# Kernel optimization log

Measured on AMD Instinct MI355X. Metric: run time of the kernel, lower is better.

## Reference

```python
import jax, jax.numpy as jnp
import numpy as np

N_NODES = 100000
N_EDGES = 1600000
IN_CH = 128
OUT_CH = 128


def setup_inputs() -> dict:
    key = jax.random.key(0)
    k1, k2, k3 = jax.random.split(key, 3)
    x = jax.random.normal(k1, (N_NODES, IN_CH), dtype=jnp.float32)
    edge_index = jax.random.randint(k2, (2, N_EDGES), 0, N_NODES, dtype=jnp.int64)
    # Glorot-style init like PyG GCNConv
    W = jax.random.normal(k3, (IN_CH, OUT_CH), dtype=jnp.float32) * (1.0 / np.sqrt(IN_CH))
    b = jnp.zeros((OUT_CH,), dtype=jnp.float32)
    return {"x": x, "edge_index": edge_index, "W": W, "b": b}


def reference(x, edge_index, W, b):
    N = x.shape[0]
    # add self-loops (PyG GCNConv default add_self_loops=True)
    loop = jnp.arange(N, dtype=edge_index.dtype)
    src = jnp.concatenate([edge_index[0], loop])
    dst = jnp.concatenate([edge_index[1], loop])
    # symmetric normalization: deg computed over destination (col)
    deg = jax.ops.segment_sum(jnp.ones_like(src, dtype=x.dtype), dst, num_segments=N)
    dinv = jnp.where(deg > 0, jax.lax.rsqrt(deg), 0.0)
    norm = dinv[src] * dinv[dst]  # [E+N]
    xw = x @ W  # [N, out_ch]
    msg = xw[src] * norm[:, None]  # gather + scale, [E+N, out_ch]
    out = jax.ops.segment_sum(msg, dst, num_segments=N) + b  # scatter-add
    return jax.nn.relu(out)
```

## Files before the change

### kernel.cpp

```cpp
#include <hip/hip_runtime.h>
#include <hip/hip_bf16.h>

constexpr int CH    = 128;
constexpr int BSH   = 7;
constexpr int CAPSH = 12;
constexpr int CHUNK = 6250;
constexpr int CHCAP = 6400;

typedef __attribute__((ext_vector_type(8))) short short8v;
typedef __attribute__((ext_vector_type(4))) float f32x4;

__device__ __forceinline__ unsigned short f2bf(float f) {
    unsigned u = __float_as_uint(f);
    u = (u + 0x7fffu + ((u >> 16) & 1u)) >> 16;
    return (unsigned short)u;
}

__global__ __launch_bounds__(256) void k_bin(const int* __restrict__ src,
                                             const int* __restrict__ dst, int E,
                                             int* __restrict__ bucket_cnt,
                                             unsigned* __restrict__ packed,
                                             const float* __restrict__ W,
                                             unsigned short* __restrict__ Wt) {
    __shared__ int hist[1024];
    __shared__ int start[1024];
    __shared__ int cursor[1024];
    __shared__ int gofs[1024];
    __shared__ int tscan[256];
    __shared__ unsigned       sorted[CHCAP];
    __shared__ unsigned short sbkt[CHCAP];

    int t = threadIdx.x;
    if (blockIdx.x < 32) {
        int idx = blockIdx.x * 256 + t;
        int c  = idx & 127;
        int k2 = (idx >> 7) * 2;
        unsigned pk = (unsigned)f2bf(W[(size_t)k2 * CH + c]) |
                      ((unsigned)f2bf(W[(size_t)(k2 + 1) * CH + c]) << 16);
        *(unsigned*)(Wt + (size_t)c * CH + k2) = pk;
    }
    #pragma unroll
    for (int i = 0; i < 4; ++i) hist[t + i * 256] = 0;
    __syncthreads();

    int e0 = blockIdx.x * CHUNK;
    int e1 = min(e0 + CHUNK, E);
    for (int e = e0 + t; e < e1; e += 256)
        atomicAdd(&hist[dst[e] >> BSH], 1);
    __syncthreads();
    int b4 = t * 4;
    int c0 = hist[b4], c1 = hist[b4 + 1], c2 = hist[b4 + 2], c3 = hist[b4 + 3];
    int tsum = c0 + c1 + c2 + c3;
    tscan[t] = tsum;
    __syncthreads();
    for (int off = 1; off < 256; off <<= 1) {
        int v = (t >= off) ? tscan[t - off] : 0;
        __syncthreads();
        tscan[t] += v;
        __syncthreads();
    }
    int eb = tscan[t] - tsum;
    start[b4]     = eb;
    start[b4 + 1] = eb + c0;
    start[b4 + 2] = eb + c0 + c1;
    start[b4 + 3] = eb + c0 + c1 + c2;
    cursor[b4]     = eb;
    cursor[b4 + 1] = eb + c0;
    cursor[b4 + 2] = eb + c0 + c1;
    cursor[b4 + 3] = eb + c0 + c1 + c2;
    __syncthreads();
    #pragma unroll
    for (int i = 0; i < 4; ++i) {
        int b = t + i * 256;
        int c = hist[b];
        gofs[b] = (c > 0) ? atomicAdd(&bucket_cnt[b], c) : 0;
    }
    __syncthreads();
    for (int e = e0 + t; e < e1; e += 256) {
        int d = dst[e];
        int b = d >> BSH;
        int pos = atomicAdd(&cursor[b], 1);
        sorted[pos] = (unsigned)src[e] | ((unsigned)(d & ((1 << BSH) - 1)) << 20);
        sbkt[pos] = (unsigned short)b;
    }
    __syncthreads();
    int nloc = e1 - e0;
    for (int i = t; i < nloc; i += 256) {
        int b = sbkt[i];
        int gpos = (b << CAPSH) + gofs[b] + (i - start[b]);
        packed[gpos] = sorted[i];
    }
}

__global__ __launch_bounds__(256) void k_bucket(const int* __restrict__ bucket_cnt,
                                                const unsigned* __restrict__ packed,
                                                int* __restrict__ eidx,
                                                uint2* __restrict__ rowinfo,
                                                float* __restrict__ dinv, int N) {
    __shared__ int fh[128];
    __shared__ int fs[128];
    __shared__ int fc[128];
    int b = blockIdx.x;
    int t = threadIdx.x;
    int cnt = bucket_cnt[b];
    if (t < 128) fh[t] = 0;
    __syncthreads();
    const unsigned* pk = packed + ((size_t)b << CAPSH);
    for (int i = t; i < cnt; i += 256)
        atomicAdd(&fh[(pk[i] >> 20) & 127], 1);
    __syncthreads();
    if (t < 128) fs[t] = fh[t];
    __syncthreads();
    for (int off = 1; off < 128; off <<= 1) {
        int v = 0;
        if (t < 128 && t >= off) v = fs[t - off];
        __syncthreads();
        if (t < 128) fs[t] += v;
        __syncthreads();
    }
    if (t < 128) {
        int excl = fs[t] - fh[t];
        fc[t] = excl;
        int node = (b << BSH) + t;
        if (node < N) {
            rowinfo[node] = make_uint2((unsigned)((b << CAPSH) + excl), (unsigned)fh[t]);
            dinv[node] = rsqrtf((float)fh[t] + 1.0f);
        }
    }
    __syncthreads();
    int* eo = eidx + ((size_t)b << CAPSH);
    for (int i = t; i < cnt; i += 256) {
        unsigned p = pk[i];
        int f = (p >> 20) & 127;
        int pos = atomicAdd(&fc[f], 1);
        eo[pos] = (int)(p & 0xFFFFF);
    }
}

__global__ __launch_bounds__(256) void k_gemm(const float* __restrict__ x,
                                              const unsigned short* __restrict__ Wt,
                                              const float* __restrict__ dinv,
                                              unsigned short* __restrict__ xwb, int N) {
    __shared__ __align__(16) unsigned short xs[64 * CH];
    int t = threadIdx.x;
    int w = t >> 6, lane = t & 63;
    int c16 = lane & 15, kq = lane >> 4, kb = kq * 8;
    int row0 = blockIdx.x * 64;
    int arow = row0 + w * 16 + c16;
    bool av = arow < N;
    const float* xp = x + (size_t)(av ? arow : 0) * CH;

    f32x4 acc[8];
    #pragma unroll
    for (int f = 0; f < 8; ++f) acc[f] = (f32x4){0.f, 0.f, 0.f, 0.f};

    #pragma unroll
    for (int kc = 0; kc < 4; ++kc) {
        float4 x0 = make_float4(0.f, 0.f, 0.f, 0.f), x1 = x0;
        if (av) {
            x0 = ((const float4*)(xp + kc * 32 + kb))[0];
            x1 = ((const float4*)(xp + kc * 32 + kb))[1];
        }
        union { short8v v; __hip_bfloat162 h[4]; } au;
        au.h[0] = __float22bfloat162_rn(make_float2(x0.x, x0.y));
        au.h[1] = __float22bfloat162_rn(make_float2(x0.z, x0.w));
        au.h[2] = __float22bfloat162_rn(make_float2(x1.x, x1.y));
        au.h[3] = __float22bfloat162_rn(make_float2(x1.z, x1.w));
        #pragma unroll
        for (int f = 0; f < 8; ++f) {
            short8v b = *(const short8v*)(Wt + (size_t)(f * 16 + c16) * CH + kc * 32 + kb);
            acc[f] = __builtin_amdgcn_mfma_f32_16x16x32_bf16(au.v, b, acc[f], 0, 0, 0);
        }
    }

    #pragma unroll
    for (int r = 0; r < 4; ++r) {
        int row_l = w * 16 + kq * 4 + r;
        int grow  = row0 + row_l;
        float dv  = (grow < N) ? dinv[grow] : 0.f;
        #pragma unroll
        for (int f = 0; f < 8; ++f) {
            int col = f * 16 + c16;
            unsigned bo = ((unsigned)((row_l * CH + col) * 2)) ^ ((unsigned)(row_l & 7) << 4);
            *(unsigned short*)((char*)xs + bo) = f2bf(acc[f][r] * dv);
        }
    }
    __syncthreads();
    #pragma unroll
    for (int i = 0; i < 4; ++i) {
        int g = i * 256 + t;
        int row_l = g >> 4;
        unsigned bo = ((unsigned)(g * 16)) ^ ((unsigned)(row_l & 7) << 4);
        uint4 v = *(const uint4*)((const char*)xs + bo);
        int row = row0 + row_l;
        if (row < N) ((uint4*)(xwb + (size_t)row * CH))[g & 15] = v;
    }
}

__global__ __launch_bounds__(256) void k_gather(const uint2* __restrict__ rowinfo,
                                                const int* __restrict__ eidx,
                                                const unsigned short* __restrict__ xwb,
                                                const float* __restrict__ dinv,
                                                const float* __restrict__ bias,
                                                float* __restrict__ out, int N) {
    int n = blockIdx.x * 4 + (threadIdx.x >> 6);
    if (n >= N) return;
    int lane = threadIdx.x & 63;
    int q    = lane >> 4;
    int c16  = lane & 15;
    uint2 ri = rowinfo[n];
    int beg = (int)ri.x;
    int deg = (int)ri.y;
    float acc[8];
    #pragma unroll
    for (int i = 0; i < 8; ++i) acc[i] = 0.f;

    const uint4* xw4 = (const uint4*)xwb;
    for (int p0 = 0; p0 < deg; p0 += 64) {
        int m = deg - p0; if (m > 64) m = 64;
        int myi = 0;
        if (lane < m) myi = eidx[beg + p0 + lane];
        int jj = q;
        int s  = (jj < m) ? __shfl(myi, jj & 63) : N;
        uint4 u = xw4[(size_t)s * 16 + c16];
        for (int j = 4; j < m; j += 4) {
            int jj2 = j + q;
            int ss  = __shfl(myi, jj2 & 63);
            int s2  = (jj2 < m) ? ss : N;
            uint4 u2 = xw4[(size_t)s2 * 16 + c16];
            acc[0] += __uint_as_float(u.x << 16);
            acc[1] += __uint_as_float(u.x & 0xffff0000u);
            acc[2] += __uint_as_float(u.y << 16);
            acc[3] += __uint_as_float(u.y & 0xffff0000u);
            acc[4] += __uint_as_float(u.z << 16);
            acc[5] += __uint_as_float(u.z & 0xffff0000u);
            acc[6] += __uint_as_float(u.w << 16);
            acc[7] += __uint_as_float(u.w & 0xffff0000u);
            u = u2;
        }
        acc[0] += __uint_as_float(u.x << 16);
        acc[1] += __uint_as_float(u.x & 0xffff0000u);
        acc[2] += __uint_as_float(u.y << 16);
        acc[3] += __uint_as_float(u.y & 0xffff0000u);
        acc[4] += __uint_as_float(u.z << 16);
        acc[5] += __uint_as_float(u.z & 0xffff0000u);
        acc[6] += __uint_as_float(u.w << 16);
        acc[7] += __uint_as_float(u.w & 0xffff0000u);
    }
    #pragma unroll
    for (int i = 0; i < 8; ++i) {
        acc[i] += __shfl_xor(acc[i], 16);
        acc[i] += __shfl_xor(acc[i], 32);
    }
    if (lane < 16) {
        float dn = dinv[n];
        uint4 u = xw4[(size_t)n * 16 + c16];
        acc[0] += __uint_as_float(u.x << 16);
        acc[1] += __uint_as_float(u.x & 0xffff0000u);
        acc[2] += __uint_as_float(u.y << 16);
        acc[3] += __uint_as_float(u.y & 0xffff0000u);
        acc[4] += __uint_as_float(u.z << 16);
        acc[5] += __uint_as_float(u.z & 0xffff0000u);
        acc[6] += __uint_as_float(u.w << 16);
        acc[7] += __uint_as_float(u.w & 0xffff0000u);
        float4 b0 = ((const float4*)bias)[c16 * 2];
        float4 b1 = ((const float4*)bias)[c16 * 2 + 1];
        float4 o0, o1;
        o0.x = fmaxf(fmaf(acc[0], dn, b0.x), 0.f);
        o0.y = fmaxf(fmaf(acc[1], dn, b0.y), 0.f);
        o0.z = fmaxf(fmaf(acc[2], dn, b0.z), 0.f);
        o0.w = fmaxf(fmaf(acc[3], dn, b0.w), 0.f);
        o1.x = fmaxf(fmaf(acc[4], dn, b1.x), 0.f);
        o1.y = fmaxf(fmaf(acc[5], dn, b1.y), 0.f);
        o1.z = fmaxf(fmaf(acc[6], dn, b1.z), 0.f);
        o1.w = fmaxf(fmaf(acc[7], dn, b1.w), 0.f);
        ((float4*)(out + (size_t)n * CH))[c16 * 2]     = o0;
        ((float4*)(out + (size_t)n * CH))[c16 * 2 + 1] = o1;
    }
}

extern "C" void kernel_launch(void* const* d_in, const int* in_sizes, int n_in,
                              void* d_out, int out_size, void* d_ws, size_t ws_size,
                              hipStream_t stream) {
    const float* x  = (const float*)d_in[0];
    const int*   ei = (const int*)d_in[1];
    const float* W  = (const float*)d_in[2];
    const float* b  = (const float*)d_in[3];

    int N = in_sizes[0] / CH;
    int E = in_sizes[1] / 2;
    const int* src = ei;
    const int* dst = ei + E;
    float* out = (float*)d_out;

    int nbuck = (N + (1 << BSH) - 1) >> BSH;
    size_t nslots = (size_t)nbuck << CAPSH;

    auto al = [](uintptr_t p) { return (p + 255) & ~(uintptr_t)255; };
    uintptr_t base = (uintptr_t)d_ws;
    unsigned short* xwb = (unsigned short*)base;
    int* bucket_cnt = (int*)(xwb + (size_t)(N + 1) * CH);
    uintptr_t p = al((uintptr_t)(bucket_cnt + nbuck));
    uint2* rowinfo  = (uint2*)p;               p = al(p + (size_t)N * 8);
    float* dinv     = (float*)p;               p = al(p + (size_t)N * 4);
    unsigned short* Wt = (unsigned short*)p;   p = al(p + (size_t)CH * CH * 2);
    unsigned* packed   = (unsigned*)p;         p = al(p + nslots * 4);
    int* eidx          = (int*)p;

    int nbin = (E + CHUNK - 1) / CHUNK;

    hipMemsetAsync(xwb + (size_t)N * CH, 0, (size_t)CH * 2 + (size_t)nbuck * 4, stream);
    k_bin   <<<nbin, 256, 0, stream>>>(src, dst, E, bucket_cnt, packed, W, Wt);
    k_bucket<<<nbuck, 256, 0, stream>>>(bucket_cnt, packed, eidx, rowinfo, dinv, N);
    k_gemm  <<<(N + 63) / 64, 256, 0, stream>>>(x, Wt, dinv, xwb, N);
    k_gather<<<(N + 3) / 4, 256, 0, stream>>>(rowinfo, eidx, xwb, dinv, b, out, N);
}
```

Before: 154.4 us.

## Split gather by column slices across blocks so each lane handles more edges

The gather kernel now splits the 128 output channels into 8 slices of 16, each handled by a separate block (blockIdx & 7). Within a wave, lane pairs cover a 16-channel slice, so 32 edges are fetched in parallel instead of 4, and each wave processes 4 nodes in sequence. The intent is to raise memory-level parallelism for the random row gathers and to use packed 2-wide float adds. The cost is that each edge index list is read 8 times, each gathered request is only 16 bytes, and the cross-lane reduction grows to 5 shuffle stages.

```diff
diff --git a/kernel.cpp b/kernel.cpp
--- a/kernel.cpp
+++ b/kernel.cpp
@@ -9,6 +9,7 @@
 
 typedef __attribute__((ext_vector_type(8))) short short8v;
 typedef __attribute__((ext_vector_type(4))) float f32x4;
+typedef __attribute__((ext_vector_type(2))) float f32x2;
 
 __device__ __forceinline__ unsigned short f2bf(float f) {
     unsigned u = __float_as_uint(f);
@@ -197,85 +198,75 @@
     }
 }
 
+#define ACCP(U) \
+    acc0 += (f32x2){__uint_as_float((U).x << 16), __uint_as_float((U).x & 0xffff0000u)}; \
+    acc1 += (f32x2){__uint_as_float((U).y << 16), __uint_as_float((U).y & 0xffff0000u)}; \
+    acc2 += (f32x2){__uint_as_float((U).z << 16), __uint_as_float((U).z & 0xffff0000u)}; \
+    acc3 += (f32x2){__uint_as_float((U).w << 16), __uint_as_float((U).w & 0xffff0000u)};
+
 __global__ __launch_bounds__(256) void k_gather(const uint2* __restrict__ rowinfo,
                                                 const int* __restrict__ eidx,
                                                 const unsigned short* __restrict__ xwb,
                                                 const float* __restrict__ dinv,
                                                 const float* __restrict__ bias,
                                                 float* __restrict__ out, int N) {
-    int n = blockIdx.x * 4 + (threadIdx.x >> 6);
-    if (n >= N) return;
-    int lane = threadIdx.x & 63;
-    int q    = lane >> 4;
-    int c16  = lane & 15;
-    uint2 ri = rowinfo[n];
-    int beg = (int)ri.x;
-    int deg = (int)ri.y;
-    float acc[8];
-    #pragma unroll
-    for (int i = 0; i < 8; ++i) acc[i] = 0.f;
-
+    int s    = blockIdx.x & 7;
+    int g    = blockIdx.x >> 3;
+    int tid  = threadIdx.x;
+    int lane = tid & 63;
+    int wv   = tid >> 6;
+    int eh   = lane >> 1;
+    int half = lane & 1;
     const uint4* xw4 = (const uint4*)xwb;
-    for (int p0 = 0; p0 < deg; p0 += 64) {
-        int m = deg - p0; if (m > 64) m = 64;
-        int myi = 0;
-        if (lane < m) myi = eidx[beg + p0 + lane];
-        int jj = q;
-        int s  = (jj < m) ? __shfl(myi, jj & 63) : N;
-        uint4 u = xw4[(size_t)s * 16 + c16];
-        for (int j = 4; j < m; j += 4) {
-            int jj2 = j + q;
-            int ss  = __shfl(myi, jj2 & 63);
-            int s2  = (jj2 < m) ? ss : N;
-            uint4 u2 = xw4[(size_t)s2 * 16 + c16];
-            acc[0] += __uint_as_float(u.x << 16);
-            acc[1] += __uint_as_float(u.x & 0xffff0000u);
-            acc[2] += __uint_as_float(u.y << 16);
-            acc[3] += __uint_as_float(u.y & 0xffff0000u);
-            acc[4] += __uint_as_float(u.z << 16);
-            acc[5] += __uint_as_float(u.z & 0xffff0000u);
-            acc[6] += __uint_as_float(u.w << 16);
-            acc[7] += __uint_as_float(u.w & 0xffff0000u);
-            u = u2;
-        }
-        acc[0] += __uint_as_float(u.x << 16);
-        acc[1] += __uint_as_float(u.x & 0xffff0000u);
-        acc[2] += __uint_as_float(u.y << 16);
-        acc[3] += __uint_as_float(u.y & 0xffff0000u);
-        acc[4] += __uint_as_float(u.z << 16);
-        acc[5] += __uint_as_float(u.z & 0xffff0000u);
-        acc[6] += __uint_as_float(u.w << 16);
-        acc[7] += __uint_as_float(u.w & 0xffff0000u);
-    }
-    #pragma unroll
-    for (int i = 0; i < 8; ++i) {
-        acc[i] += __shfl_xor(acc[i], 16);
-        acc[i] += __shfl_xor(acc[i], 32);
-    }
-    if (lane < 16) {
-        float dn = dinv[n];
-        uint4 u = xw4[(size_t)n * 16 + c16];
-        acc[0] += __uint_as_float(u.x << 16);
-        acc[1] += __uint_as_float(u.x & 0xffff0000u);
-        acc[2] += __uint_as_float(u.y << 16);
-        acc[3] += __uint_as_float(u.y & 0xffff0000u);
-        acc[4] += __uint_as_float(u.z << 16);
-        acc[5] += __uint_as_float(u.z & 0xffff0000u);
-        acc[6] += __uint_as_float(u.w << 16);
-        acc[7] += __uint_as_float(u.w & 0xffff0000u);
-        float4 b0 = ((const float4*)bias)[c16 * 2];
-        float4 b1 = ((const float4*)bias)[c16 * 2 + 1];
-        float4 o0, o1;
-        o0.x = fmaxf(fmaf(acc[0], dn, b0.x), 0.f);
-        o0.y = fmaxf(fmaf(acc[1], dn, b0.y), 0.f);
-        o0.z = fmaxf(fmaf(acc[2], dn, b0.z), 0.f);
-        o0.w = fmaxf(fmaf(acc[3], dn, b0.w), 0.f);
-        o1.x = fmaxf(fmaf(acc[4], dn, b1.x), 0.f);
-        o1.y = fmaxf(fmaf(acc[5], dn, b1.y), 0.f);
-        o1.z = fmaxf(fmaf(acc[6], dn, b1.z), 0.f);
-        o1.w = fmaxf(fmaf(acc[7], dn, b1.w), 0.f);
-        ((float4*)(out + (size_t)n * CH))[c16 * 2]     = o0;
-        ((float4*)(out + (size_t)n * CH))[c16 * 2 + 1] = o1;
+    int sb = s * 2 + half;
+
+    float4 b0 = ((const float4*)bias)[s * 4 + half * 2];
+    float4 b1 = ((const float4*)bias)[s * 4 + half * 2 + 1];
+
+    #pragma unroll
+    for (int i = 0; i < 4; ++i) {
+        int n = g * 16 + wv * 4 + i;
+        if (n >= N) break;
+        uint2 ri = rowinfo[n];
+        int beg = (int)ri.x;
+        int deg = (int)ri.y;
+        f32x2 acc0 = {0.f, 0.f}, acc1 = {0.f, 0.f}, acc2 = {0.f, 0.f}, acc3 = {0.f, 0.f};
+        for (int p0 = 0; p0 < deg; p0 += 64) {
+            int m = deg - p0; if (m > 64) m = 64;
+            int myi = 0;
+            if (lane < m) myi = eidx[beg + p0 + lane];
+            for (int j = 0; j < m; j += 32) {
+                int e = j + eh;
+                int a = __shfl(myi, e);
+                int srow = (e < m) ? a : N;
+                uint4 u = xw4[(size_t)srow * 16 + sb];
+                ACCP(u);
+            }
+        }
+        #pragma unroll
+        for (int st = 2; st <= 32; st <<= 1) {
+            acc0.x += __shfl_xor(acc0.x, st);  acc0.y += __shfl_xor(acc0.y, st);
+            acc1.x += __shfl_xor(acc1.x, st);  acc1.y += __shfl_xor(acc1.y, st);
+            acc2.x += __shfl_xor(acc2.x, st);  acc2.y += __shfl_xor(acc2.y, st);
+            acc3.x += __shfl_xor(acc3.x, st);  acc3.y += __shfl_xor(acc3.y, st);
+        }
+        if (eh == 0) {
+            float dn = dinv[n];
+            uint4 u = xw4[(size_t)n * 16 + sb];
+            ACCP(u);
+            float4 o0, o1;
+            o0.x = fmaxf(fmaf(acc0.x, dn, b0.x), 0.f);
+            o0.y = fmaxf(fmaf(acc0.y, dn, b0.y), 0.f);
+            o0.z = fmaxf(fmaf(acc1.x, dn, b0.z), 0.f);
+            o0.w = fmaxf(fmaf(acc1.y, dn, b0.w), 0.f);
+            o1.x = fmaxf(fmaf(acc2.x, dn, b1.x), 0.f);
+            o1.y = fmaxf(fmaf(acc2.y, dn, b1.y), 0.f);
+            o1.z = fmaxf(fmaf(acc3.x, dn, b1.z), 0.f);
+            o1.w = fmaxf(fmaf(acc3.y, dn, b1.w), 0.f);
+            float* op = out + (size_t)n * CH + s * 16 + half * 8;
+            ((float4*)op)[0] = o0;
+            ((float4*)op)[1] = o1;
+        }
     }
 }
 
@@ -313,5 +304,8 @@
     k_bin   <<<nbin, 256, 0, stream>>>(src, dst, E, bucket_cnt, packed, W, Wt);
     k_bucket<<<nbuck, 256, 0, stream>>>(bucket_cnt, packed, eidx, rowinfo, dinv, N);
     k_gemm  <<<(N + 63) / 64, 256, 0, stream>>>(x, Wt, dinv, xwb, N);
-    k_gather<<<(N + 3) / 4, 256, 0, stream>>>(rowinfo, eidx, xwb, dinv, b, out, N);
-}
+    {
+        int ngrp = (N + 15) / 16;
+        k_gather<<<ngrp * 8, 256, 0, stream>>>(rowinfo, eidx, xwb, dinv, b, out, N);
+    }
+}
```

Result: slower. 423.0 us (+173.9%).
